# Kernel tuning notes

Hardware: AMD Instinct MI355X
Metric: run time of the kernel (lower is better)

## Reference

```python
import jax, jax.numpy as jnp
import numpy as np

EMB_DIM = 64
B, S, D = 64, 1024, 64

def setup_inputs() -> dict:
    key = jax.random.key(0)
    k1, k2, k3, k4, k5 = jax.random.split(key, 5)
    return {
        "query": jax.random.normal(k1, (B, S, D), dtype=jnp.float32),
        "key": jax.random.normal(k2, (B, S, D), dtype=jnp.float32),
        "value": jax.random.normal(k3, (B, S, D), dtype=jnp.float32),
        "a_key": jax.random.normal(k4, (S, S, D), dtype=jnp.float32),
        "a_value": jax.random.normal(k5, (S, S, D), dtype=jnp.float32),
    }

def reference(query, key, value, a_key, a_value):
    scale = jnp.sqrt(jnp.asarray(EMB_DIM, dtype=query.dtype))
    # standard content-content scores: [B, Sq, Sk]
    qk = jnp.einsum("bqd,bkd->bqk", query, key)
    # relative key scores: a_key is [Sq, Sk, D]; contract over D per query position
    rel_qk = jnp.einsum("bqd,qkd->bqk", query, a_key)
    attn = jax.nn.softmax((qk + rel_qk) / scale, axis=-1)
    # content values + relative values
    qkv = jnp.einsum("bqk,bkd->bqd", attn, value)
    rel_qkv = jnp.einsum("bqk,qkd->bqd", attn, a_value)
    return qkv + rel_qkv, attn
```

## Files before the change

### kernel.cpp

```cpp
#include <hip/hip_runtime.h>
#include <stdint.h>

#define S_ 1024
#define D_ 64
#define B_ 64

typedef short short8 __attribute__((ext_vector_type(8)));
typedef unsigned short ushort8 __attribute__((ext_vector_type(8)));
typedef float f32x4 __attribute__((ext_vector_type(4)));

__device__ __forceinline__ unsigned short f2bf(float x) {
    uint32_t u = __builtin_bit_cast(uint32_t, x);
    return (unsigned short)((u + 0x7FFFu + ((u >> 16) & 1u)) >> 16);
}
__device__ __forceinline__ float bf2f(unsigned short b) {
    return __builtin_bit_cast(float, ((uint32_t)b) << 16);
}
__device__ __forceinline__ uint32_t pack2(float a, float b) {
    return (uint32_t)f2bf(a) | ((uint32_t)f2bf(b) << 16);
}
__device__ __forceinline__ int scidx(int row, int k) {
    return (((row << 10) + (k & ~7)) ^ ((row & 15) << 3)) + (k & 7);
}

__global__ __launch_bounds__(256) void k1_qk(const float* __restrict__ Q,
                                             const float* __restrict__ Kk,
                                             float* __restrict__ qk) {
    __shared__ __align__(16) unsigned short Qs[128][72];
    __shared__ __align__(16) unsigned short Ks[128][72];
    const float SCL = 0.18033688011112042f;
    const int bx = blockIdx.x;
    const int b  = bx >> 6;
    const int q0 = ((bx >> 3) & 7) << 7;
    const int k0 = (bx & 7) << 7;
    const int t  = threadIdx.x;
#pragma unroll
    for (int i = 0; i < 8; ++i) {
        int f = (i << 8) + t;
        int row = f >> 4, c = (f & 15) << 2;
        float4 v = *reinterpret_cast<const float4*>(&Q[((size_t)(b * S_ + q0 + row) << 6) + c]);
        *reinterpret_cast<uint2*>(&Qs[row][c]) = make_uint2(pack2(v.x, v.y), pack2(v.z, v.w));
        float4 u = *reinterpret_cast<const float4*>(&Kk[((size_t)(b * S_ + k0 + row) << 6) + c]);
        *reinterpret_cast<uint2*>(&Ks[row][c]) = make_uint2(pack2(u.x, u.y), pack2(u.z, u.w));
    }
    __syncthreads();
    const int l = t & 63, w = t >> 6, lr = l & 15, lg = l >> 4;
    short8 a[2][2];
#pragma unroll
    for (int mi = 0; mi < 2; ++mi)
#pragma unroll
        for (int h = 0; h < 2; ++h)
            a[mi][h] = *reinterpret_cast<const short8*>(&Qs[((w * 2 + mi) << 4) + lr][h * 32 + lg * 8]);
    f32x4 acc[2][8] = {};
#pragma unroll
    for (int n = 0; n < 8; ++n) {
        short8 b0 = *reinterpret_cast<const short8*>(&Ks[(n << 4) + lr][lg * 8]);
        short8 b1 = *reinterpret_cast<const short8*>(&Ks[(n << 4) + lr][32 + lg * 8]);
#pragma unroll
        for (int mi = 0; mi < 2; ++mi) {
            acc[mi][n] = __builtin_amdgcn_mfma_f32_16x16x32_bf16(a[mi][0], b0, acc[mi][n], 0, 0, 0);
            acc[mi][n] = __builtin_amdgcn_mfma_f32_16x16x32_bf16(a[mi][1], b1, acc[mi][n], 0, 0, 0);
        }
    }
#pragma unroll
    for (int mi = 0; mi < 2; ++mi)
#pragma unroll
        for (int n = 0; n < 8; ++n)
#pragma unroll
            for (int r = 0; r < 4; ++r) {
                int qq = q0 + ((w * 2 + mi) << 4) + (lg << 2) + r;
                int kc = k0 + (n << 4) + lr;
                qk[((size_t)(b * S_ + qq) << 10) + kc] = acc[mi][n][r] * SCL;
            }
}

__device__ __forceinline__ void tpose_store_p(unsigned short* Tls, int pitch, float4 p,
                                              int kb, int t) {
    const int l = t & 63, lr = l & 15, lg = l >> 4;
    float v0 = p.x, v1 = p.y, v2 = p.z, v3 = p.w;
    float y0 = __shfl_xor(v0, 16), y1 = __shfl_xor(v1, 16),
          y2 = __shfl_xor(v2, 16), y3 = __shfl_xor(v3, 16);
    bool o = (lg & 1);
    float n0 = o ? y1 : v0, n1 = o ? v1 : y0, n2 = o ? y3 : v2, n3 = o ? v3 : y2;
    float z0 = __shfl_xor(n0, 32), z1 = __shfl_xor(n1, 32),
          z2 = __shfl_xor(n2, 32), z3 = __shfl_xor(n3, 32);
    bool h = (lg & 2);
    float T0 = h ? z2 : n0, T1 = h ? z3 : n1, T2 = h ? n2 : z0, T3 = h ? n3 : z1;
    int d = (lr << 2) + lg;
    *reinterpret_cast<uint2*>(&Tls[d * pitch + kb]) = make_uint2(pack2(T0, T1), pack2(T2, T3));
}

__global__ __launch_bounds__(512) void k2_mid(const float* __restrict__ Q,
                                              const float* __restrict__ AK,
                                              const float* __restrict__ AV,
                                              float* __restrict__ attn,
                                              float* __restrict__ outp) {
    __shared__ __align__(16) unsigned short Sc[64 * 1024];
    __shared__ __align__(16) unsigned short Qs[64][72];
    __shared__ __align__(16) unsigned short Ak[2][64][72];
    __shared__ float invs[64];
    const float SCL = 0.18033688011112042f;
    const int q = blockIdx.x;
    const int t = threadIdx.x;
    const int l = t & 63, w = t >> 6, lr = l & 15, lg = l >> 4;
    const int wq = w & 3;
    const int wh = w >> 2;
    const int srow = t >> 3, sc8 = (t & 7) << 3;

    {
        const float* qp = &Q[((size_t)(srow * S_ + q) << 6) + sc8];
        float4 a = *reinterpret_cast<const float4*>(qp);
        float4 b = *reinterpret_cast<const float4*>(qp + 4);
        *reinterpret_cast<uint4*>(&Qs[srow][sc8]) =
            make_uint4(pack2(a.x * SCL, a.y * SCL), pack2(a.z * SCL, a.w * SCL),
                       pack2(b.x * SCL, b.y * SCL), pack2(b.z * SCL, b.w * SCL));
    }
    const float* akbase = &AK[(size_t)q << 16];
    float4 pa[2][2];
#define LDK(set, tile) do { const float* p_ = akbase + ((size_t)(tile) << 12) + (srow << 6) + sc8; \
        pa[set][0] = *reinterpret_cast<const float4*>(p_);                                         \
        pa[set][1] = *reinterpret_cast<const float4*>(p_ + 4); } while (0)
#define STAGEK(buf) do {                                                                     \
        *reinterpret_cast<uint4*>(&Ak[buf][srow][sc8]) =                                     \
            make_uint4(pack2(pa[buf][0].x, pa[buf][0].y), pack2(pa[buf][0].z, pa[buf][0].w), \
                       pack2(pa[buf][1].x, pa[buf][1].y), pack2(pa[buf][1].z, pa[buf][1].w)); } while (0)
    LDK(0, 0); LDK(1, 1);
    __syncthreads();
    short8 qa[2][2];
#pragma unroll
    for (int bh = 0; bh < 2; ++bh)
#pragma unroll
        for (int h = 0; h < 2; ++h)
            qa[bh][h] = *reinterpret_cast<const short8*>(
                &Qs[(wh << 5) + (bh << 4) + lr][(h << 5) + (lg << 3)]);
    STAGEK(0);
    __syncthreads();

#pragma unroll 2
    for (int tt = 0; tt < 16; ++tt) {
        const int cur = tt & 1, nxt = cur ^ 1;
        short8 ak0 = *reinterpret_cast<const short8*>(&Ak[cur][(wq << 4) + lr][lg << 3]);
        short8 ak1 = *reinterpret_cast<const short8*>(&Ak[cur][(wq << 4) + lr][32 + (lg << 3)]);
        if (tt < 15) STAGEK(nxt);
        if (tt < 14) LDK(cur, tt + 2);
        int kbase = (tt << 6) + (wq << 4) + (lg << 2);
#pragma unroll
        for (int bh = 0; bh < 2; ++bh) {
            f32x4 c = {};
            c = __builtin_amdgcn_mfma_f32_16x16x32_bf16(ak0, qa[bh][0], c, 0, 0, 0);
            c = __builtin_amdgcn_mfma_f32_16x16x32_bf16(ak1, qa[bh][1], c, 0, 0, 0);
            *reinterpret_cast<uint2*>(&Sc[scidx((wh << 5) + (bh << 4) + lr, kbase)]) =
                make_uint2(pack2(c[0], c[1]), pack2(c[2], c[3]));
        }
        __syncthreads();
    }
#undef LDK
#undef STAGEK

    const float* avbase = &AV[(size_t)q << 16];
    float4 pv[2][2];
#pragma unroll
    for (int s = 0; s < 2; ++s)
#pragma unroll
        for (int i = 0; i < 2; ++i) {
            int f = (i << 9) + t;
            pv[s][i] = *reinterpret_cast<const float4*>(
                &avbase[((size_t)s << 12) + ((size_t)(f >> 4) << 6) + ((f & 15) << 2)]);
        }

    {
        const int ch = t & 7;
        const float* qkrow = &attn[((size_t)(srow * S_ + q) << 10)];
        float s = 0.f;
#pragma unroll 4
        for (int i = 0; i < 16; ++i) {
            int k = (((i << 3) + ch) << 3);
            float4 g0 = *reinterpret_cast<const float4*>(&qkrow[k]);
            float4 g1 = *reinterpret_cast<const float4*>(&qkrow[k + 4]);
            int idx = scidx(srow, k);
            ushort8 rel = *reinterpret_cast<const ushort8*>(&Sc[idx]);
            float p0 = exp2f(g0.x + bf2f(rel[0]));
            float p1 = exp2f(g0.y + bf2f(rel[1]));
            float p2 = exp2f(g0.z + bf2f(rel[2]));
            float p3 = exp2f(g0.w + bf2f(rel[3]));
            float p4 = exp2f(g1.x + bf2f(rel[4]));
            float p5 = exp2f(g1.y + bf2f(rel[5]));
            float p6 = exp2f(g1.z + bf2f(rel[6]));
            float p7 = exp2f(g1.w + bf2f(rel[7]));
            s += ((p0 + p1) + (p2 + p3)) + ((p4 + p5) + (p6 + p7));
            ushort8 e;
            e[0] = f2bf(p0); e[1] = f2bf(p1); e[2] = f2bf(p2); e[3] = f2bf(p3);
            e[4] = f2bf(p4); e[5] = f2bf(p5); e[6] = f2bf(p6); e[7] = f2bf(p7);
            *reinterpret_cast<ushort8*>(&Sc[idx]) = e;
        }
        s += __shfl_xor(s, 1); s += __shfl_xor(s, 2); s += __shfl_xor(s, 4);
        if (ch == 0) invs[srow] = 1.0f / s;
    }
    __syncthreads();

    tpose_store_p(&Ak[0][0][0], 72, pv[0][0], (w << 2), t);
    tpose_store_p(&Ak[0][0][0], 72, pv[0][1], 32 + (w << 2), t);
    __syncthreads();

    f32x4 oacc[2] = {};
#pragma unroll 2
    for (int tt = 0; tt < 16; ++tt) {
        const int cur = tt & 1, nxt = cur ^ 1;
        short8 bb0 = *reinterpret_cast<const short8*>(&Ak[cur][(wq << 4) + lr][lg << 3]);
        short8 bb1 = *reinterpret_cast<const short8*>(&Ak[cur][(wq << 4) + lr][32 + (lg << 3)]);
        if (tt < 15) {
            tpose_store_p(&Ak[nxt][0][0], 72, pv[nxt][0], (w << 2), t);
            tpose_store_p(&Ak[nxt][0][0], 72, pv[nxt][1], 32 + (w << 2), t);
        }
        if (tt < 14) {
#pragma unroll
            for (int i = 0; i < 2; ++i) {
                int f = (i << 9) + t;
                pv[cur][i] = *reinterpret_cast<const float4*>(
                    &avbase[((size_t)(tt + 2) << 12) + ((size_t)(f >> 4) << 6) + ((f & 15) << 2)]);
            }
        }
        {
            int col = (t & 255) << 2;
#pragma unroll
            for (int rr = 0; rr < 2; ++rr) {
                int row = (tt << 2) + (rr << 1) + wh;
                uint2 u = *reinterpret_cast<const uint2*>(&Sc[scidx(row, col)]);
                float inv = invs[row];
                float4 o = make_float4(bf2f((unsigned short)(u.x & 0xffff)) * inv,
                                       bf2f((unsigned short)(u.x >> 16)) * inv,
                                       bf2f((unsigned short)(u.y & 0xffff)) * inv,
                                       bf2f((unsigned short)(u.y >> 16)) * inv);
                *reinterpret_cast<float4*>(&attn[((size_t)(row * S_ + q) << 10) + col]) = o;
            }
        }
#pragma unroll
        for (int mi = 0; mi < 2; ++mi) {
            short8 ea0 = *reinterpret_cast<const short8*>(
                &Sc[scidx((wh << 5) + (mi << 4) + lr, (tt << 6) + (lg << 3))]);
            short8 ea1 = *reinterpret_cast<const short8*>(
                &Sc[scidx((wh << 5) + (mi << 4) + lr, (tt << 6) + 32 + (lg << 3))]);
            oacc[mi] = __builtin_amdgcn_mfma_f32_16x16x32_bf16(ea0, bb0, oacc[mi], 0, 0, 0);
            oacc[mi] = __builtin_amdgcn_mfma_f32_16x16x32_bf16(ea1, bb1, oacc[mi], 0, 0, 0);
        }
        __syncthreads();
    }
#pragma unroll
    for (int mi = 0; mi < 2; ++mi)
#pragma unroll
        for (int r = 0; r < 4; ++r) {
            int brow = (wh << 5) + (mi << 4) + (lg << 2) + r;
            outp[((size_t)(brow * S_ + q) << 6) + (wq << 4) + lr] = oacc[mi][r] * invs[brow];
        }
}

__global__ __launch_bounds__(512) void k3_pv(const float* __restrict__ V,
                                             const float* __restrict__ attn,
                                             float* __restrict__ outp) {
    __shared__ __align__(16) unsigned short Vt[64 * 1032];
    __shared__ __align__(16) unsigned short At[2][64][72];
    const int b  = blockIdx.x >> 2;
    const int qq = blockIdx.x & 3;
    const int t  = threadIdx.x;
    const int l = t & 63, w = t >> 6, lr = l & 15, lg = l >> 4;
    const int wq = w & 3;
    const int dh = w >> 2;
    const int srow = t >> 3, sc8 = (t & 7) << 3;

    for (int kt = 0; kt < 16; ++kt) {
#pragma unroll
        for (int i = 0; i < 2; ++i) {
            int f = (i << 9) + t;
            int row = f >> 4, c = (f & 15) << 2;
            float4 pvv = *reinterpret_cast<const float4*>(
                &V[((size_t)(b * S_ + (kt << 6) + row) << 6) + c]);
            tpose_store_p(&Vt[0], 1032, pvv, (kt << 6) + (i << 5) + (w << 2), t);
        }
    }
    __syncthreads();

    for (int qs = 0; qs < 4; ++qs) {
        const float* arow = &attn[((size_t)((b * S_ + (qq << 8) + (qs << 6) + srow)) << 10) + sc8];
        float4 pa[2][2];
#define LDA3(set, tile) do { const float* p_ = arow + ((tile) << 6);       \
        pa[set][0] = *reinterpret_cast<const float4*>(p_);                 \
        pa[set][1] = *reinterpret_cast<const float4*>(p_ + 4); } while (0)
#define STAGEA(buf) do {                                                                     \
        *reinterpret_cast<uint4*>(&At[buf][srow][sc8]) =                                     \
            make_uint4(pack2(pa[buf][0].x, pa[buf][0].y), pack2(pa[buf][0].z, pa[buf][0].w), \
                       pack2(pa[buf][1].x, pa[buf][1].y), pack2(pa[buf][1].z, pa[buf][1].w)); } while (0)
        LDA3(0, 0); LDA3(1, 1);
        __syncthreads();
        STAGEA(0);
        __syncthreads();
        f32x4 acc[2] = {};
#pragma unroll 2
        for (int kt = 0; kt < 16; ++kt) {
            const int cur = kt & 1, nxt = cur ^ 1;
            short8 a0 = *reinterpret_cast<const short8*>(&At[cur][(wq << 4) + lr][lg << 3]);
            short8 a1 = *reinterpret_cast<const short8*>(&At[cur][(wq << 4) + lr][32 + (lg << 3)]);
            if (kt < 15) STAGEA(nxt);
            if (kt < 14) LDA3(cur, kt + 2);
#pragma unroll
            for (int n = 0; n < 2; ++n) {
                const unsigned short* vb = &Vt[((dh << 5) + (n << 4) + lr) * 1032 + (kt << 6) + (lg << 3)];
                short8 b0 = *reinterpret_cast<const short8*>(vb);
                short8 b1 = *reinterpret_cast<const short8*>(vb + 32);
                acc[n] = __builtin_amdgcn_mfma_f32_16x16x32_bf16(a0, b0, acc[n], 0, 0, 0);
                acc[n] = __builtin_amdgcn_mfma_f32_16x16x32_bf16(a1, b1, acc[n], 0, 0, 0);
            }
            __syncthreads();
        }
#undef LDA3
#undef STAGEA
#pragma unroll
        for (int n = 0; n < 2; ++n)
#pragma unroll
            for (int r = 0; r < 4; ++r) {
                size_t idx = ((size_t)(b * S_ + (qq << 8) + (qs << 6) + (wq << 4) + (lg << 2) + r) << 6)
                             + (dh << 5) + (n << 4) + lr;
                outp[idx] += acc[n][r];
            }
    }
}

extern "C" void kernel_launch(void* const* d_in, const int* in_sizes, int n_in,
                              void* d_out, int out_size, void* d_ws, size_t ws_size,
                              hipStream_t stream) {
    (void)in_sizes; (void)n_in; (void)out_size; (void)d_ws; (void)ws_size;
    const float* Q  = (const float*)d_in[0];
    const float* K  = (const float*)d_in[1];
    const float* V  = (const float*)d_in[2];
    const float* AK = (const float*)d_in[3];
    const float* AV = (const float*)d_in[4];
    float* outp = (float*)d_out;
    float* attn = outp + (size_t)B_ * S_ * D_;

    k1_qk <<<dim3(64 * 8 * 8), dim3(256), 0, stream>>>(Q, K, attn);
    k2_mid<<<dim3(1024),       dim3(512), 0, stream>>>(Q, AK, AV, attn, outp);
    k3_pv <<<dim3(256),        dim3(512), 0, stream>>>(V, attn, outp);
}
```

Baseline: 405.6 us.

## Load MFMA operands directly from global into registers, dropping LDS staging and barriers

In k2_mid's a_key score phase and in k3_pv's attention-tile loop, each lane now reads its MFMA A-fragment straight from global memory into registers and packs it to bf16 there. The shared-memory staging buffers and the per-tile __syncthreads are removed. In k2_mid the work is redistributed: each half of the block takes 8 of the 16 key tiles for all 64 batch rows, instead of all tiles for half the rows. This cuts LDS round-trips and barrier stalls, but the per-lane global loads are less coalesced (32-byte strided chunks) and register pressure rises because more Q fragments are held.

```diff
diff --git a/kernel.cpp b/kernel.cpp
--- a/kernel.cpp
+++ b/kernel.cpp
@@ -18,6 +18,12 @@
 }
 __device__ __forceinline__ uint32_t pack2(float a, float b) {
     return (uint32_t)f2bf(a) | ((uint32_t)f2bf(b) << 16);
+}
+__device__ __forceinline__ short8 mkfrag(float4 a, float4 b) {
+    union { short8 s; uint32_t u[4]; } r;
+    r.u[0] = pack2(a.x, a.y); r.u[1] = pack2(a.z, a.w);
+    r.u[2] = pack2(b.x, b.y); r.u[3] = pack2(b.z, b.w);
+    return r.s;
 }
 __device__ __forceinline__ int scidx(int row, int k) {
     return (((row << 10) + (k & ~7)) ^ ((row & 15) << 3)) + (k & 7);
@@ -104,7 +110,7 @@
     const int t = threadIdx.x;
     const int l = t & 63, w = t >> 6, lr = l & 15, lg = l >> 4;
     const int wq = w & 3;
-    const int wh = w >> 2;
+    const int th = w >> 2;
     const int srow = t >> 3, sc8 = (t & 7) << 3;
 
     {
@@ -115,47 +121,43 @@
             make_uint4(pack2(a.x * SCL, a.y * SCL), pack2(a.z * SCL, a.w * SCL),
                        pack2(b.x * SCL, b.y * SCL), pack2(b.z * SCL, b.w * SCL));
     }
-    const float* akbase = &AK[(size_t)q << 16];
-    float4 pa[2][2];
-#define LDK(set, tile) do { const float* p_ = akbase + ((size_t)(tile) << 12) + (srow << 6) + sc8; \
-        pa[set][0] = *reinterpret_cast<const float4*>(p_);                                         \
-        pa[set][1] = *reinterpret_cast<const float4*>(p_ + 4); } while (0)
-#define STAGEK(buf) do {                                                                     \
-        *reinterpret_cast<uint4*>(&Ak[buf][srow][sc8]) =                                     \
-            make_uint4(pack2(pa[buf][0].x, pa[buf][0].y), pack2(pa[buf][0].z, pa[buf][0].w), \
-                       pack2(pa[buf][1].x, pa[buf][1].y), pack2(pa[buf][1].z, pa[buf][1].w)); } while (0)
-    LDK(0, 0); LDK(1, 1);
-    __syncthreads();
-    short8 qa[2][2];
-#pragma unroll
-    for (int bh = 0; bh < 2; ++bh)
+    __syncthreads();
+    short8 qa[4][2];
+#pragma unroll
+    for (int bh = 0; bh < 4; ++bh)
 #pragma unroll
         for (int h = 0; h < 2; ++h)
             qa[bh][h] = *reinterpret_cast<const short8*>(
-                &Qs[(wh << 5) + (bh << 4) + lr][(h << 5) + (lg << 3)]);
-    STAGEK(0);
-    __syncthreads();
-
+                &Qs[(bh << 4) + lr][(h << 5) + (lg << 3)]);
+
+    {
+        const float* base = &AK[((size_t)q << 16) + (((wq << 4) + lr) << 6) + (lg << 3)];
+        float4 A0[2], A1[2], A2[2], A3[2];
+#define LDA(buf, i8) do { const float* p_ = base + ((size_t)((th << 3) + (i8)) << 12); \
+        A0[buf] = *reinterpret_cast<const float4*>(p_);                                \
+        A1[buf] = *reinterpret_cast<const float4*>(p_ + 4);                            \
+        A2[buf] = *reinterpret_cast<const float4*>(p_ + 32);                           \
+        A3[buf] = *reinterpret_cast<const float4*>(p_ + 36); } while (0)
+        LDA(0, 0); LDA(1, 1);
 #pragma unroll 2
-    for (int tt = 0; tt < 16; ++tt) {
-        const int cur = tt & 1, nxt = cur ^ 1;
-        short8 ak0 = *reinterpret_cast<const short8*>(&Ak[cur][(wq << 4) + lr][lg << 3]);
-        short8 ak1 = *reinterpret_cast<const short8*>(&Ak[cur][(wq << 4) + lr][32 + (lg << 3)]);
-        if (tt < 15) STAGEK(nxt);
-        if (tt < 14) LDK(cur, tt + 2);
-        int kbase = (tt << 6) + (wq << 4) + (lg << 2);
-#pragma unroll
-        for (int bh = 0; bh < 2; ++bh) {
-            f32x4 c = {};
-            c = __builtin_amdgcn_mfma_f32_16x16x32_bf16(ak0, qa[bh][0], c, 0, 0, 0);
-            c = __builtin_amdgcn_mfma_f32_16x16x32_bf16(ak1, qa[bh][1], c, 0, 0, 0);
-            *reinterpret_cast<uint2*>(&Sc[scidx((wh << 5) + (bh << 4) + lr, kbase)]) =
-                make_uint2(pack2(c[0], c[1]), pack2(c[2], c[3]));
-        }
-        __syncthreads();
-    }
-#undef LDK
-#undef STAGEK
+        for (int i8 = 0; i8 < 8; ++i8) {
+            const int buf = i8 & 1;
+            short8 ak0 = mkfrag(A0[buf], A1[buf]);
+            short8 ak1 = mkfrag(A2[buf], A3[buf]);
+            if (i8 < 6) LDA(buf, i8 + 2);
+            int kbase = (((th << 3) + i8) << 6) + (wq << 4) + (lg << 2);
+#pragma unroll
+            for (int bh = 0; bh < 4; ++bh) {
+                f32x4 c = {};
+                c = __builtin_amdgcn_mfma_f32_16x16x32_bf16(ak0, qa[bh][0], c, 0, 0, 0);
+                c = __builtin_amdgcn_mfma_f32_16x16x32_bf16(ak1, qa[bh][1], c, 0, 0, 0);
+                *reinterpret_cast<uint2*>(&Sc[scidx((bh << 4) + lr, kbase)]) =
+                    make_uint2(pack2(c[0], c[1]), pack2(c[2], c[3]));
+            }
+        }
+#undef LDA
+    }
+    __syncthreads();
 
     const float* avbase = &AV[(size_t)q << 16];
     float4 pv[2][2];
@@ -224,7 +226,7 @@
             int col = (t & 255) << 2;
 #pragma unroll
             for (int rr = 0; rr < 2; ++rr) {
-                int row = (tt << 2) + (rr << 1) + wh;
+                int row = (tt << 2) + (rr << 1) + th;
                 uint2 u = *reinterpret_cast<const uint2*>(&Sc[scidx(row, col)]);
                 float inv = invs[row];
                 float4 o = make_float4(bf2f((unsigned short)(u.x & 0xffff)) * inv,
@@ -237,9 +239,9 @@
 #pragma unroll
         for (int mi = 0; mi < 2; ++mi) {
             short8 ea0 = *reinterpret_cast<const short8*>(
-                &Sc[scidx((wh << 5) + (mi << 4) + lr, (tt << 6) + (lg << 3))]);
+                &Sc[scidx((th << 5) + (mi << 4) + lr, (tt << 6) + (lg << 3))]);
             short8 ea1 = *reinterpret_cast<const short8*>(
-                &Sc[scidx((wh << 5) + (mi << 4) + lr, (tt << 6) + 32 + (lg << 3))]);
+                &Sc[scidx((th << 5) + (mi << 4) + lr, (tt << 6) + 32 + (lg << 3))]);
             oacc[mi] = __builtin_amdgcn_mfma_f32_16x16x32_bf16(ea0, bb0, oacc[mi], 0, 0, 0);
             oacc[mi] = __builtin_amdgcn_mfma_f32_16x16x32_bf16(ea1, bb1, oacc[mi], 0, 0, 0);
         }
@@ -249,7 +251,7 @@
     for (int mi = 0; mi < 2; ++mi)
 #pragma unroll
         for (int r = 0; r < 4; ++r) {
-            int brow = (wh << 5) + (mi << 4) + (lg << 2) + r;
+            int brow = (th << 5) + (mi << 4) + (lg << 2) + r;
             outp[((size_t)(brow * S_ + q) << 6) + (wq << 4) + lr] = oacc[mi][r] * invs[brow];
         }
 }
@@ -258,14 +260,12 @@
                                              const float* __restrict__ attn,
                                              float* __restrict__ outp) {
     __shared__ __align__(16) unsigned short Vt[64 * 1032];
-    __shared__ __align__(16) unsigned short At[2][64][72];
     const int b  = blockIdx.x >> 2;
     const int qq = blockIdx.x & 3;
     const int t  = threadIdx.x;
     const int l = t & 63, w = t >> 6, lr = l & 15, lg = l >> 4;
     const int wq = w & 3;
     const int dh = w >> 2;
-    const int srow = t >> 3, sc8 = (t & 7) << 3;
 
     for (int kt = 0; kt < 16; ++kt) {
 #pragma unroll
@@ -280,27 +280,21 @@
     __syncthreads();
 
     for (int qs = 0; qs < 4; ++qs) {
-        const float* arow = &attn[((size_t)((b * S_ + (qq << 8) + (qs << 6) + srow)) << 10) + sc8];
-        float4 pa[2][2];
-#define LDA3(set, tile) do { const float* p_ = arow + ((tile) << 6);       \
-        pa[set][0] = *reinterpret_cast<const float4*>(p_);                 \
-        pa[set][1] = *reinterpret_cast<const float4*>(p_ + 4); } while (0)
-#define STAGEA(buf) do {                                                                     \
-        *reinterpret_cast<uint4*>(&At[buf][srow][sc8]) =                                     \
-            make_uint4(pack2(pa[buf][0].x, pa[buf][0].y), pack2(pa[buf][0].z, pa[buf][0].w), \
-                       pack2(pa[buf][1].x, pa[buf][1].y), pack2(pa[buf][1].z, pa[buf][1].w)); } while (0)
-        LDA3(0, 0); LDA3(1, 1);
-        __syncthreads();
-        STAGEA(0);
-        __syncthreads();
+        const float* arow = &attn[((size_t)((b * S_ + (qq << 8) + (qs << 6) + (wq << 4) + lr)) << 10) + (lg << 3)];
+        float4 A0[2], A1[2], A2[2], A3[2];
+#define LDP(buf, kt) do { const float* p_ = arow + ((kt) << 6);        \
+        A0[buf] = *reinterpret_cast<const float4*>(p_);                \
+        A1[buf] = *reinterpret_cast<const float4*>(p_ + 4);            \
+        A2[buf] = *reinterpret_cast<const float4*>(p_ + 32);           \
+        A3[buf] = *reinterpret_cast<const float4*>(p_ + 36); } while (0)
+        LDP(0, 0); LDP(1, 1);
         f32x4 acc[2] = {};
 #pragma unroll 2
         for (int kt = 0; kt < 16; ++kt) {
-            const int cur = kt & 1, nxt = cur ^ 1;
-            short8 a0 = *reinterpret_cast<const short8*>(&At[cur][(wq << 4) + lr][lg << 3]);
-            short8 a1 = *reinterpret_cast<const short8*>(&At[cur][(wq << 4) + lr][32 + (lg << 3)]);
-            if (kt < 15) STAGEA(nxt);
-            if (kt < 14) LDA3(cur, kt + 2);
+            const int buf = kt & 1;
+            short8 a0 = mkfrag(A0[buf], A1[buf]);
+            short8 a1 = mkfrag(A2[buf], A3[buf]);
+            if (kt < 14) LDP(buf, kt + 2);
 #pragma unroll
             for (int n = 0; n < 2; ++n) {
                 const unsigned short* vb = &Vt[((dh << 5) + (n << 4) + lr) * 1032 + (kt << 6) + (lg << 3)];
@@ -309,10 +303,8 @@
                 acc[n] = __builtin_amdgcn_mfma_f32_16x16x32_bf16(a0, b0, acc[n], 0, 0, 0);
                 acc[n] = __builtin_amdgcn_mfma_f32_16x16x32_bf16(a1, b1, acc[n], 0, 0, 0);
             }
-            __syncthreads();
-        }
-#undef LDA3
-#undef STAGEA
+        }
+#undef LDP
 #pragma unroll
         for (int n = 0; n < 2; ++n)
 #pragma unroll
```

Result: slower. 415.0 us (+2.3%).
